# Kernel tuning notes

Hardware: AMD Instinct MI355X
Metric: run time of the kernel (lower is better)

## Reference

```python
import jax, jax.numpy as jnp
import numpy as np

B, T, C, H = 256, 256, 384, 64  # batch, seq (== block_size), n_embd, head_size


def setup_inputs() -> dict:
    key = jax.random.key(0)
    kx, kk, kq, kv = jax.random.split(key, 4)
    scale = C ** -0.5
    x = jax.random.normal(kx, (B, T, C), dtype=jnp.float32)
    Wk = jax.random.normal(kk, (C, H), dtype=jnp.float32) * scale
    Wq = jax.random.normal(kq, (C, H), dtype=jnp.float32) * scale
    Wv = jax.random.normal(kv, (C, H), dtype=jnp.float32) * scale
    return {"x": x, "Wk": Wk, "Wq": Wq, "Wv": Wv}


def reference(x, Wk, Wq, Wv):
    # Single causal self-attention head (x_kv=None path). Dropout is eval-mode (identity).
    Tn = x.shape[1]
    k = x @ Wk            # [B, T, H]
    q = x @ Wq            # [B, T, H]
    v = x @ Wv            # [B, T, H]
    inv_sqrt_d = k.shape[-1] ** -0.5
    wei = jnp.einsum('bth,bsh->bts', q, k) * inv_sqrt_d  # [B, T, T]
    causal = jnp.tril(jnp.ones((Tn, Tn), dtype=bool))
    wei = jnp.where(causal, wei, -jnp.inf)
    wei = jax.nn.softmax(wei, axis=-1)
    out = jnp.einsum('bts,bsh->bth', wei, v)             # [B, T, H]
    return out
```

## Files before the change

kernel.cpp:

```cpp
#include <hip/hip_runtime.h>

#define BATCH 256
#define SEQ   256
#define CDIM  384
#define HDIM  64

typedef __attribute__((ext_vector_type(8))) short bf16x8;
typedef __attribute__((ext_vector_type(4))) float f32x4;

__device__ __forceinline__ unsigned f2bf(float f) {
  union { float f; unsigned u; } v; v.f = f;
  unsigned r = v.u + 0x7FFFu + ((v.u >> 16) & 1u);
  return r >> 16;
}

__global__ void wtrans_kernel(const float* __restrict__ Wk, const float* __restrict__ Wq,
                              const float* __restrict__ Wv, unsigned short* __restrict__ WTf) {
  int gid = blockIdx.x * 256 + threadIdx.x;
  if (gid >= 192 * CDIM) return;
  int n = gid / CDIM, kk = gid - n * CDIM;
  const float* W = (n < 64) ? Wq : (n < 128) ? Wk : Wv;
  int nt = n >> 4, ln = n & 15, ks = kk >> 5, sub = (kk >> 3) & 3, j = kk & 7;
  int lane = ln + 16 * sub;
  WTf[(((size_t)ks * 12 + nt) * 64 + lane) * 8 + j] =
      (unsigned short)f2bf(W[kk * HDIM + (n & 63)]);
}

__global__ __launch_bounds__(512, 2) void fused_kernel(
    const float* __restrict__ x, const unsigned short* __restrict__ WTf,
    float* __restrict__ out) {
  __shared__ __align__(16) unsigned short lds[73728];
  const int tid = threadIdx.x, b = blockIdx.x;
  const int w = tid >> 6, lane = tid & 63;
  const int ln15 = lane & 15, quad = lane >> 4;

  {
    #pragma unroll
    for (int i = 0; i < 18; ++i) {
      int c = i * 512 + tid;
      __builtin_amdgcn_global_load_lds(
          (const __attribute__((address_space(1))) unsigned*)((const char*)WTf + (size_t)c * 16),
          (__attribute__((address_space(3))) unsigned*)((char*)lds + (size_t)c * 16),
          16, 0, 0);
    }
  }
  __builtin_amdgcn_sched_barrier(0);

  const float* xr = x + (size_t)(b * 256 + w * 32 + ln15) * CDIM + quad * 8;

  float4 P0[12], P1[12];

#define LOADST(BUF, BASE)                                                    \
  {                                                                          \
    _Pragma("unroll")                                                        \
    for (int j = 0; j < 3; ++j) {                                            \
      BUF[4 * j]     = *(const float4*)(xr + ((BASE) + j) * 32);             \
      BUF[4 * j + 1] = *(const float4*)(xr + ((BASE) + j) * 32 + 4);         \
      BUF[4 * j + 2] = *(const float4*)(xr + 16 * CDIM + ((BASE) + j) * 32); \
      BUF[4 * j + 3] = *(const float4*)(xr + 16 * CDIM + ((BASE) + j) * 32 + 4); \
    }                                                                        \
  }

#define USEST(BUF, BASE)                                                     \
  {                                                                          \
    _Pragma("unroll")                                                        \
    for (int k2 = 0; k2 < 3; ++k2) {                                         \
      float4 a0 = BUF[4 * k2],     a1 = BUF[4 * k2 + 1];                     \
      float4 c0 = BUF[4 * k2 + 2], c1 = BUF[4 * k2 + 3];                     \
      bf16x8 t0, t1;                                                         \
      t0[0] = (short)f2bf(a0.x); t0[1] = (short)f2bf(a0.y);                  \
      t0[2] = (short)f2bf(a0.z); t0[3] = (short)f2bf(a0.w);                  \
      t0[4] = (short)f2bf(a1.x); t0[5] = (short)f2bf(a1.y);                  \
      t0[6] = (short)f2bf(a1.z); t0[7] = (short)f2bf(a1.w);                  \
      t1[0] = (short)f2bf(c0.x); t1[1] = (short)f2bf(c0.y);                  \
      t1[2] = (short)f2bf(c0.z); t1[3] = (short)f2bf(c0.w);                  \
      t1[4] = (short)f2bf(c1.x); t1[5] = (short)f2bf(c1.y);                  \
      t1[6] = (short)f2bf(c1.z); t1[7] = (short)f2bf(c1.w);                  \
      _Pragma("unroll")                                                      \
      for (int nt = 0; nt < 12; ++nt) {                                      \
        bf16x8 aw = *(const bf16x8*)&lds[((((BASE) + k2) * 12 + nt) * 64 + lane) * 8]; \
        acc0[nt] = __builtin_amdgcn_mfma_f32_16x16x32_bf16(aw, t0, acc0[nt], 0, 0, 0); \
        acc1[nt] = __builtin_amdgcn_mfma_f32_16x16x32_bf16(aw, t1, acc1[nt], 0, 0, 0); \
      }                                                                      \
    }                                                                        \
  }

  LOADST(P0, 0)
  __builtin_amdgcn_sched_barrier(0);

  asm volatile("s_waitcnt vmcnt(12)" ::: "memory");
  __builtin_amdgcn_s_barrier();
  __builtin_amdgcn_sched_barrier(0);

  f32x4 acc0[12], acc1[12];
  #pragma unroll
  for (int nt = 0; nt < 12; ++nt) {
    acc0[nt] = (f32x4){0.f, 0.f, 0.f, 0.f};
    acc1[nt] = (f32x4){0.f, 0.f, 0.f, 0.f};
  }

  LOADST(P1, 3)
  USEST(P0, 0)
  LOADST(P0, 6)
  USEST(P1, 3)
  LOADST(P1, 9)
  USEST(P0, 6)
  USEST(P1, 9)

  __syncthreads();

  unsigned short (*QL)[72]  = (unsigned short(*)[72])lds;
  unsigned short (*KL)[72]  = (unsigned short(*)[72])(lds + 18432);
  unsigned short (*VT)[264] = (unsigned short(*)[264])(lds + 36864);
  unsigned short (*PL)[36]  = (unsigned short(*)[36])(lds + 53760 + w * 576);

#define HANDOFF(ACC, TROW)                                                   \
  {                                                                          \
    _Pragma("unroll")                                                        \
    for (int nt = 0; nt < 4; ++nt) {                                         \
      f32x4 a = ACC[nt];                                                     \
      unsigned p0 = f2bf(a[0]) | (f2bf(a[1]) << 16);                         \
      unsigned p1 = f2bf(a[2]) | (f2bf(a[3]) << 16);                         \
      *(uint2*)&QL[TROW][nt * 16 + quad * 4] = (uint2){p0, p1};              \
    }                                                                        \
    _Pragma("unroll")                                                        \
    for (int nt = 4; nt < 8; ++nt) {                                         \
      f32x4 a = ACC[nt];                                                     \
      unsigned p0 = f2bf(a[0]) | (f2bf(a[1]) << 16);                         \
      unsigned p1 = f2bf(a[2]) | (f2bf(a[3]) << 16);                         \
      *(uint2*)&KL[TROW][(nt - 4) * 16 + quad * 4] = (uint2){p0, p1};        \
    }                                                                        \
    _Pragma("unroll")                                                        \
    for (int nt = 8; nt < 12; ++nt) {                                        \
      f32x4 a = ACC[nt];                                                     \
      const int h = (nt - 8) * 16 + quad * 4;                                \
      _Pragma("unroll")                                                      \
      for (int i = 0; i < 4; ++i)                                            \
        VT[h + i][TROW] = (unsigned short)f2bf(a[i]);                        \
    }                                                                        \
  }

  {
    const int trow0 = w * 32 + ln15;
    const int trow1 = trow0 + 16;
    HANDOFF(acc0, trow0)
    HANDOFF(acc1, trow1)
  }
  __syncthreads();

  for (int mi = 0; mi < 2; ++mi) {
    const int mt = mi ? (15 - w) : w;
    const int t0 = mt * 16;
    const int NT = (mt | 1) + 1;

    bf16x8 aq[2];
    #pragma unroll
    for (int ks = 0; ks < 2; ++ks)
      aq[ks] = *(const bf16x8*)&QL[t0 + ln15][ks * 32 + quad * 8];

    float sv[16][4];
    #pragma unroll
    for (int nt = 0; nt < 16; ++nt) {
      if (nt < NT) {
        f32x4 a2 = (f32x4){0.f, 0.f, 0.f, 0.f};
        #pragma unroll
        for (int ks = 0; ks < 2; ++ks) {
          bf16x8 bf = *(const bf16x8*)&KL[nt * 16 + ln15][ks * 32 + quad * 8];
          a2 = __builtin_amdgcn_mfma_f32_16x16x32_bf16(aq[ks], bf, a2, 0, 0, 0);
        }
        int colg = nt * 16 + ln15;
        #pragma unroll
        for (int i = 0; i < 4; ++i) {
          int rowg = t0 + quad * 4 + i;
          sv[nt][i] = (colg <= rowg) ? a2[i] * 0.125f : -3.0e38f;
        }
      }
    }
    float mx[4] = {-3.0e38f, -3.0e38f, -3.0e38f, -3.0e38f};
    #pragma unroll
    for (int nt = 0; nt < 16; ++nt)
      if (nt < NT) {
        #pragma unroll
        for (int i = 0; i < 4; ++i) mx[i] = fmaxf(mx[i], sv[nt][i]);
      }
    #pragma unroll
    for (int i = 0; i < 4; ++i) {
      mx[i] = fmaxf(mx[i], __shfl_xor(mx[i], 8, 64));
      mx[i] = fmaxf(mx[i], __shfl_xor(mx[i], 4, 64));
      mx[i] = fmaxf(mx[i], __shfl_xor(mx[i], 2, 64));
      mx[i] = fmaxf(mx[i], __shfl_xor(mx[i], 1, 64));
    }
    float sm[4] = {0.f, 0.f, 0.f, 0.f};
    #pragma unroll
    for (int nt = 0; nt < 16; ++nt)
      if (nt < NT) {
        #pragma unroll
        for (int i = 0; i < 4; ++i) {
          float e = __expf(sv[nt][i] - mx[i]);
          sv[nt][i] = e;
          sm[i] += e;
        }
      }
    #pragma unroll
    for (int i = 0; i < 4; ++i) {
      sm[i] += __shfl_xor(sm[i], 8, 64);
      sm[i] += __shfl_xor(sm[i], 4, 64);
      sm[i] += __shfl_xor(sm[i], 2, 64);
      sm[i] += __shfl_xor(sm[i], 1, 64);
    }
    float inv[4];
    #pragma unroll
    for (int i = 0; i < 4; ++i) inv[i] = 1.0f / sm[i];

    f32x4 o[4];
    #pragma unroll
    for (int ont = 0; ont < 4; ++ont) o[ont] = (f32x4){0.f, 0.f, 0.f, 0.f};

    #pragma unroll
    for (int kc = 0; kc < 8; ++kc) {
      if (kc * 2 < NT) {
        #pragma unroll
        for (int half = 0; half < 2; ++half) {
          int nt = kc * 2 + half;
          #pragma unroll
          for (int i = 0; i < 4; ++i)
            PL[quad * 4 + i][half * 16 + ln15] =
                (unsigned short)f2bf(sv[nt][i] * inv[i]);
        }
        bf16x8 pa = *(const bf16x8*)&PL[ln15][quad * 8];
        #pragma unroll
        for (int ont = 0; ont < 4; ++ont) {
          bf16x8 vb = *(const bf16x8*)&VT[ont * 16 + ln15][kc * 32 + quad * 8];
          o[ont] = __builtin_amdgcn_mfma_f32_16x16x32_bf16(pa, vb, o[ont], 0, 0, 0);
        }
      }
    }

    #pragma unroll
    for (int ont = 0; ont < 4; ++ont) {
      int h = ont * 16 + ln15;
      #pragma unroll
      for (int i = 0; i < 4; ++i)
        out[(size_t)(b * 256 + t0 + quad * 4 + i) * HDIM + h] = o[ont][i];
    }
  }
}

extern "C" void kernel_launch(void* const* d_in, const int* in_sizes, int n_in,
                              void* d_out, int out_size, void* d_ws, size_t ws_size,
                              hipStream_t stream) {
  const float* x  = (const float*)d_in[0];
  const float* Wk = (const float*)d_in[1];
  const float* Wq = (const float*)d_in[2];
  const float* Wv = (const float*)d_in[3];
  float* out = (float*)d_out;

  unsigned short* WTf = (unsigned short*)d_ws;

  wtrans_kernel<<<(192 * CDIM + 255) / 256, 256, 0, stream>>>(Wk, Wq, Wv, WTf);
  fused_kernel<<<256, 512, 0, stream>>>(x, WTf, out);
}
```

Baseline: 172.5 us.

## Stream x through swizzled LDS double buffers via DMA and split weight staging

Replaces the register-prefetched x loads with per-wave global_load_lds DMA into a double-buffered LDS region, using an XOR swizzle so the later LDS reads avoid bank conflicts. Each k-step issues the next chunk's DMA and waits only on the older one, so loading overlaps the MFMA work. The projection weights are now staged in two halves, with a block-wide barrier and reload partway through the projection. This frees registers and LDS, but adds per-step vmcnt waits and a mid-loop synchronisation stall.

```diff
diff --git a/kernel.cpp b/kernel.cpp
--- a/kernel.cpp
+++ b/kernel.cpp
@@ -29,68 +29,50 @@
 __global__ __launch_bounds__(512, 2) void fused_kernel(
     const float* __restrict__ x, const unsigned short* __restrict__ WTf,
     float* __restrict__ out) {
-  __shared__ __align__(16) unsigned short lds[73728];
+  __shared__ __align__(16) char L[139264];
   const int tid = threadIdx.x, b = blockIdx.x;
   const int w = tid >> 6, lane = tid & 63;
   const int ln15 = lane & 15, quad = lane >> 4;
 
   {
     #pragma unroll
-    for (int i = 0; i < 18; ++i) {
-      int c = i * 512 + tid;
+    for (int i = 0; i < 9; ++i) {
+      int rec = w * 9 + i;
       __builtin_amdgcn_global_load_lds(
-          (const __attribute__((address_space(1))) unsigned*)((const char*)WTf + (size_t)c * 16),
-          (__attribute__((address_space(3))) unsigned*)((char*)lds + (size_t)c * 16),
+          (const __attribute__((address_space(1))) unsigned*)((const char*)WTf + (size_t)rec * 1024 + lane * 16),
+          (__attribute__((address_space(3))) unsigned*)(L + (size_t)rec * 1024 + lane * 16),
           16, 0, 0);
     }
   }
   __builtin_amdgcn_sched_barrier(0);
 
-  const float* xr = x + (size_t)(b * 256 + w * 32 + ln15) * CDIM + quad * 8;
-
-  float4 P0[12], P1[12];
-
-#define LOADST(BUF, BASE)                                                    \
-  {                                                                          \
-    _Pragma("unroll")                                                        \
-    for (int j = 0; j < 3; ++j) {                                            \
-      BUF[4 * j]     = *(const float4*)(xr + ((BASE) + j) * 32);             \
-      BUF[4 * j + 1] = *(const float4*)(xr + ((BASE) + j) * 32 + 4);         \
-      BUF[4 * j + 2] = *(const float4*)(xr + 16 * CDIM + ((BASE) + j) * 32); \
-      BUF[4 * j + 3] = *(const float4*)(xr + 16 * CDIM + ((BASE) + j) * 32 + 4); \
-    }                                                                        \
-  }
-
-#define USEST(BUF, BASE)                                                     \
-  {                                                                          \
-    _Pragma("unroll")                                                        \
-    for (int k2 = 0; k2 < 3; ++k2) {                                         \
-      float4 a0 = BUF[4 * k2],     a1 = BUF[4 * k2 + 1];                     \
-      float4 c0 = BUF[4 * k2 + 2], c1 = BUF[4 * k2 + 3];                     \
-      bf16x8 t0, t1;                                                         \
-      t0[0] = (short)f2bf(a0.x); t0[1] = (short)f2bf(a0.y);                  \
-      t0[2] = (short)f2bf(a0.z); t0[3] = (short)f2bf(a0.w);                  \
-      t0[4] = (short)f2bf(a1.x); t0[5] = (short)f2bf(a1.y);                  \
-      t0[6] = (short)f2bf(a1.z); t0[7] = (short)f2bf(a1.w);                  \
-      t1[0] = (short)f2bf(c0.x); t1[1] = (short)f2bf(c0.y);                  \
-      t1[2] = (short)f2bf(c0.z); t1[3] = (short)f2bf(c0.w);                  \
-      t1[4] = (short)f2bf(c1.x); t1[5] = (short)f2bf(c1.y);                  \
-      t1[6] = (short)f2bf(c1.z); t1[7] = (short)f2bf(c1.w);                  \
-      _Pragma("unroll")                                                      \
-      for (int nt = 0; nt < 12; ++nt) {                                      \
-        bf16x8 aw = *(const bf16x8*)&lds[((((BASE) + k2) * 12 + nt) * 64 + lane) * 8]; \
-        acc0[nt] = __builtin_amdgcn_mfma_f32_16x16x32_bf16(aw, t0, acc0[nt], 0, 0, 0); \
-        acc1[nt] = __builtin_amdgcn_mfma_f32_16x16x32_bf16(aw, t1, acc1[nt], 0, 0, 0); \
-      }                                                                      \
-    }                                                                        \
-  }
-
-  LOADST(P0, 0)
-  __builtin_amdgcn_sched_barrier(0);
-
-  asm volatile("s_waitcnt vmcnt(12)" ::: "memory");
+  const int r0 = lane >> 3;
+  const int cgs = (lane & 7) ^ r0;
+  const char* xsrc = (const char*)x +
+      ((size_t)(b * 256 + w * 32 + r0) * CDIM + cgs * 4) * 4;
+  char* xbuf = L + 73728 + w * 8192;
+
+#define XDMA(K, S)                                                            \
+  {                                                                           \
+    _Pragma("unroll")                                                         \
+    for (int j = 0; j < 4; ++j) {                                             \
+      __builtin_amdgcn_global_load_lds(                                       \
+          (const __attribute__((address_space(1))) unsigned*)(xsrc +          \
+              (size_t)j * 8 * CDIM * 4 + (K) * 128),                          \
+          (__attribute__((address_space(3))) unsigned*)(xbuf + (S) * 4096 +   \
+              j * 1024 + lane * 16),                                          \
+          16, 0, 0);                                                          \
+    }                                                                         \
+  }
+
+  XDMA(0, 0)
+  __builtin_amdgcn_sched_barrier(0);
+  asm volatile("s_waitcnt vmcnt(4)" ::: "memory");
   __builtin_amdgcn_s_barrier();
   __builtin_amdgcn_sched_barrier(0);
+
+  const int roA = ln15 * 128 + (((2 * quad) ^ (ln15 & 7)) * 16);
+  const int roB = ln15 * 128 + ((((2 * quad) + 1) ^ (ln15 & 7)) * 16);
 
   f32x4 acc0[12], acc1[12];
   #pragma unroll
@@ -99,20 +81,70 @@
     acc1[nt] = (f32x4){0.f, 0.f, 0.f, 0.f};
   }
 
-  LOADST(P1, 3)
-  USEST(P0, 0)
-  LOADST(P0, 6)
-  USEST(P1, 3)
-  LOADST(P1, 9)
-  USEST(P0, 6)
-  USEST(P1, 9)
+#define PSTEP(K, KIDX, VMN, ISSUE)                                            \
+  {                                                                           \
+    ISSUE                                                                     \
+    __builtin_amdgcn_sched_barrier(0);                                        \
+    asm volatile("s_waitcnt vmcnt(" #VMN ")" ::: "memory");                   \
+    __builtin_amdgcn_sched_barrier(0);                                        \
+    const char* cb = xbuf + ((K) & 1) * 4096;                                 \
+    float4 fa0 = *(const float4*)(cb + roA);                                  \
+    float4 fb0 = *(const float4*)(cb + roB);                                  \
+    float4 fa1 = *(const float4*)(cb + 2048 + roA);                           \
+    float4 fb1 = *(const float4*)(cb + 2048 + roB);                           \
+    bf16x8 t0, t1;                                                            \
+    t0[0] = (short)f2bf(fa0.x); t0[1] = (short)f2bf(fa0.y);                   \
+    t0[2] = (short)f2bf(fa0.z); t0[3] = (short)f2bf(fa0.w);                   \
+    t0[4] = (short)f2bf(fb0.x); t0[5] = (short)f2bf(fb0.y);                   \
+    t0[6] = (short)f2bf(fb0.z); t0[7] = (short)f2bf(fb0.w);                   \
+    t1[0] = (short)f2bf(fa1.x); t1[1] = (short)f2bf(fa1.y);                   \
+    t1[2] = (short)f2bf(fa1.z); t1[3] = (short)f2bf(fa1.w);                   \
+    t1[4] = (short)f2bf(fb1.x); t1[5] = (short)f2bf(fb1.y);                   \
+    t1[6] = (short)f2bf(fb1.z); t1[7] = (short)f2bf(fb1.w);                   \
+    _Pragma("unroll")                                                         \
+    for (int nt = 0; nt < 12; ++nt) {                                         \
+      bf16x8 aw = *(const bf16x8*)(L + ((KIDX) * 12 + nt) * 1024 + lane * 16); \
+      acc0[nt] = __builtin_amdgcn_mfma_f32_16x16x32_bf16(aw, t0, acc0[nt], 0, 0, 0); \
+      acc1[nt] = __builtin_amdgcn_mfma_f32_16x16x32_bf16(aw, t1, acc1[nt], 0, 0, 0); \
+    }                                                                         \
+  }
+
+  PSTEP(0, 0, 4, XDMA(1, 1))
+  PSTEP(1, 1, 4, XDMA(2, 0))
+  PSTEP(2, 2, 4, XDMA(3, 1))
+  PSTEP(3, 3, 4, XDMA(4, 0))
+  PSTEP(4, 4, 4, XDMA(5, 1))
+  PSTEP(5, 5, 4, XDMA(6, 0))
+
+  __builtin_amdgcn_sched_barrier(0);
+  __builtin_amdgcn_s_barrier();
+  {
+    #pragma unroll
+    for (int i = 0; i < 9; ++i) {
+      int rec = w * 9 + i;
+      __builtin_amdgcn_global_load_lds(
+          (const __attribute__((address_space(1))) unsigned*)((const char*)WTf + 73728 + (size_t)rec * 1024 + lane * 16),
+          (__attribute__((address_space(3))) unsigned*)(L + (size_t)rec * 1024 + lane * 16),
+          16, 0, 0);
+    }
+  }
+  asm volatile("s_waitcnt vmcnt(0)" ::: "memory");
+  __builtin_amdgcn_s_barrier();
+  __builtin_amdgcn_sched_barrier(0);
+
+  PSTEP(6,  0, 4, XDMA(7, 1))
+  PSTEP(7,  1, 4, XDMA(8, 0))
+  PSTEP(8,  2, 4, XDMA(9, 1))
+  PSTEP(9,  3, 4, XDMA(10, 0))
+  PSTEP(10, 4, 4, XDMA(11, 1))
+  PSTEP(11, 5, 0, )
 
   __syncthreads();
 
-  unsigned short (*QL)[72]  = (unsigned short(*)[72])lds;
-  unsigned short (*KL)[72]  = (unsigned short(*)[72])(lds + 18432);
-  unsigned short (*VT)[264] = (unsigned short(*)[264])(lds + 36864);
-  unsigned short (*PL)[36]  = (unsigned short(*)[36])(lds + 53760 + w * 576);
+  unsigned short (*QL)[72]  = (unsigned short(*)[72])L;
+  unsigned short (*KL)[72]  = (unsigned short(*)[72])(L + 36864);
+  unsigned short (*VT)[264] = (unsigned short(*)[264])(L + 73728);
+  unsigned short (*PL)[36]  = (unsigned short(*)[36])(L + 107520 + w * 1152);
 
 #define HANDOFF(ACC, TROW)                                                   \
   {                                                                          \
```

Result: no change. 172.2 us (-0.2%).
